# Performance work log

Measured on AMD Instinct MI355X. Metric: run time of the kernel, lower is better.

Reference implementation:

```python
import jax, jax.numpy as jnp
import numpy as np

SNUM = 8           # number of select-PUF stages
PUF_LEN = 64       # arbiter PUF length -> phi dim = PUF_LEN + 1
BATCH = 262144     # number of challenge-response pairs
D = 2 ** SNUM      # 256 combinations


def _make_kron_tables():
    """Replicates the W/B kron construction from combineMPUF.__init__.
    Returns Wmat, Bmat of shape [SNUM, D]; row i is W[i]/B[i] (originally [1, D])."""
    tmpX = np.array([[1], [1]])
    Ws, Bs = [], []
    for i in range(SNUM):
        w = np.array([[-1], [1]])
        b = np.array([[1], [0]])
        for _ in range(i + 1, SNUM):
            w = np.kron(tmpX, w)
            b = np.kron(tmpX, b)
        for _ in range(i):
            w = np.kron(w, tmpX)
            b = np.kron(b, tmpX)
        Ws.append(w.T[0])
        Bs.append(b.T[0])
    return (jnp.asarray(np.stack(Ws), jnp.float32),
            jnp.asarray(np.stack(Bs), jnp.float32))


def setup_inputs() -> dict:
    key = jax.random.key(0)
    k_phi, k_ws, k_bs, k_wd, k_bd = jax.random.split(key, 5)
    F = PUF_LEN + 1
    scale = 1.0 / np.sqrt(F)  # ~ torch Linear init scale
    phi = jax.random.normal(k_phi, (BATCH, F), dtype=jnp.float32)
    W_S = jax.random.uniform(k_ws, (SNUM, F), jnp.float32, -scale, scale)
    b_S = jax.random.uniform(k_bs, (SNUM,), jnp.float32, -scale, scale)
    W_D = jax.random.uniform(k_wd, (D, F), jnp.float32, -scale, scale)
    b_D = jax.random.uniform(k_bd, (D,), jnp.float32, -scale, scale)
    Wmat, Bmat = _make_kron_tables()
    return {"phi": phi, "W_S": W_S, "b_S": b_S, "W_D": W_D, "b_D": b_D,
            "Wmat": Wmat, "Bmat": Bmat}


def reference(phi, W_S, b_S, W_D, b_D, Wmat, Bmat):
    # phi: [B, F]; W_S: [SNUM, F]; W_D: [D, F]; Wmat/Bmat: [SNUM, D]
    Sdelta = phi @ W_S.T + b_S            # [B, SNUM]
    Ddelta = phi @ W_D.T + b_D            # [B, D]
    Souts = jax.nn.sigmoid(Sdelta)        # [B, SNUM]
    Douts = jax.nn.sigmoid(Ddelta)        # [B, D]
    # sigmoid-gated outer-product chain: M = prod_i (s_i * w_i + b_i)
    M = jnp.ones_like(Douts)
    for i in range(SNUM):                 # small fixed structural loop
        M = M * (Souts[:, i:i + 1] * Wmat[i] + Bmat[i])
    ans = jnp.sum(Douts * M * 0.99999, axis=-1, keepdims=True)  # [B, 1]
    reliability_output = jnp.abs(Sdelta)  # [B, SNUM]
    return ans, reliability_output
```

## Files before the change

kernel.cpp:

```cpp
#include <hip/hip_runtime.h>

typedef float  f32x4  __attribute__((ext_vector_type(4)));
typedef float  f32x4a __attribute__((ext_vector_type(4), aligned(4)));
typedef float  f32x2  __attribute__((ext_vector_type(2)));
typedef __bf16 bf16x8 __attribute__((ext_vector_type(8)));
typedef short  short8 __attribute__((ext_vector_type(8)));

#define F      65
#define NTT    17
#define KS3    3
#define RPB    128
#define NCHUNK (NTT*KS3*64)

__device__ __forceinline__ unsigned short f2bf(float f) {
  unsigned int u = __builtin_bit_cast(unsigned int, f);
  u += 0x7FFFu + ((u >> 16) & 1u);
  return (unsigned short)(u >> 16);
}
__device__ __forceinline__ float fast_sigmoid(float x) {
  float e = __builtin_amdgcn_exp2f(-1.4426950408889634f * x);
  return __builtin_amdgcn_rcpf(1.0f + e);
}
template<int CTRL>
__device__ __forceinline__ float dpp_mov(float v) {
  return __builtin_bit_cast(float,
    __builtin_amdgcn_update_dpp(0, __builtin_bit_cast(int, v), CTRL, 0xF, 0xF, true));
}

__global__ void prep_w(const float* __restrict__ W_S, const float* __restrict__ b_S,
                       const float* __restrict__ W_D, const float* __restrict__ b_D,
                       unsigned short* __restrict__ wsb) {
  int b = blockIdx.x;
  int t = b / 3, s = b % 3;
  int l = threadIdx.x;
  int c = l & 15, q = l >> 4;
  short8 out;
#pragma unroll
  for (int j = 0; j < 8; ++j) {
    int k = 32 * s + 8 * q + j;
    float v = 0.0f;
    if (t < 16) {
      int n = 16 * t + c;
      if (k < F)       v = W_D[n * F + k];
      else if (k == F) v = b_D[n];
    } else if (c < 8) {
      if (k < F)       v = W_S[c * F + k];
      else if (k == F) v = b_S[c];
    }
    out[j] = (short)f2bf(v);
  }
  reinterpret_cast<short8*>(wsb)[b * 64 + l] = out;
}

__launch_bounds__(512, 4)
__global__ void mpuf_main(const float* __restrict__ phi,
                          const unsigned short* __restrict__ wsb,
                          float* __restrict__ out_ans,
                          float* __restrict__ out_rel) {
  __shared__ short8 ldsB[NCHUNK];
  __shared__ float  soutv[RPB][10];
  __shared__ float  rowrec[RPB][18];

  const int tid  = threadIdx.x;
  const int wave = tid >> 6;
  const int l    = tid & 63;
  const int c    = l & 15;
  const int q    = l >> 4;
  const int wrow = wave * 16;
  const int brow = blockIdx.x * RPB;

  const float* prow = phi + (size_t)(brow + wrow + c) * F;

  f32x4a f4[4];
#pragma unroll
  for (int s = 0; s < 2; ++s) {
    f4[2 * s]     = *reinterpret_cast<const f32x4a*>(prow + 32 * s + 8 * q);
    f4[2 * s + 1] = *reinterpret_cast<const f32x4a*>(prow + 32 * s + 8 * q + 4);
  }
  const float a64 = prow[64];

  const short8* wsv = reinterpret_cast<const short8*>(wsb);
#pragma unroll
  for (int i = 0; i < 7; ++i) {
    int idx = tid + i * 512;
    if (idx < NCHUNK) ldsB[idx] = wsv[idx];
  }

  bf16x8 af[3];
#pragma unroll
  for (int s = 0; s < 2; ++s) {
    short8 ar;
#pragma unroll
    for (int j = 0; j < 4; ++j) {
      ar[j]     = (short)f2bf(f4[2 * s][j]);
      ar[j + 4] = (short)f2bf(f4[2 * s + 1][j]);
    }
    af[s] = __builtin_bit_cast(bf16x8, ar);
  }
  {
    short8 ar = {0, 0, 0, 0, 0, 0, 0, 0};
    if (q == 0) {
      ar[0] = (short)f2bf(a64);
      ar[1] = (short)0x3F80;
    }
    af[2] = __builtin_bit_cast(bf16x8, ar);
  }

  __syncthreads();

  f32x4 accS = {};
#pragma unroll
  for (int s = 0; s < KS3; ++s)
    accS = __builtin_amdgcn_mfma_f32_16x16x32_bf16(
               af[s], __builtin_bit_cast(bf16x8, ldsB[(16 * KS3 + s) * 64 + l]),
               accS, 0, 0, 0);

  if (c < 8) {
#pragma unroll
    for (int r = 0; r < 4; ++r) {
      const int R = wrow + q * 4 + r;
      float sd = accS[r];
      out_rel[(size_t)(brow + R) * 8 + c] = fabsf(sd);
      soutv[R][c] = fast_sigmoid(sd);
    }
  }

  float Ml[4];
#pragma unroll
  for (int r = 0; r < 4; ++r) {
    const int R = wrow + q * 4 + r;
    f32x2 p01 = *reinterpret_cast<const f32x2*>(&soutv[R][0]);
    f32x2 p23 = *reinterpret_cast<const f32x2*>(&soutv[R][2]);
    f32x2 p45 = *reinterpret_cast<const f32x2*>(&soutv[R][4]);
    f32x2 p67 = *reinterpret_cast<const f32x2*>(&soutv[R][6]);
    float m = 0.99999f;
    m *= (c & 1) ? p01[0] : 1.0f - p01[0];
    m *= (c & 2) ? p01[1] : 1.0f - p01[1];
    m *= (c & 4) ? p23[0] : 1.0f - p23[0];
    m *= (c & 8) ? p23[1] : 1.0f - p23[1];
    Ml[r] = m;
    float mt = (c & 1) ? p45[0] : 1.0f - p45[0];
    mt *= (c & 2) ? p45[1] : 1.0f - p45[1];
    mt *= (c & 4) ? p67[0] : 1.0f - p67[0];
    mt *= (c & 8) ? p67[1] : 1.0f - p67[1];
    rowrec[R][c] = mt;
  }

  float ansacc[4] = {0.0f, 0.0f, 0.0f, 0.0f};

#pragma unroll 1
  for (int tp = 0; tp < 8; ++tp) {
    const int t0 = 2 * tp, t1 = t0 + 1;
    f32x4 A0 = {}, A1 = {};
#pragma unroll
    for (int s = 0; s < KS3; ++s)
      A0 = __builtin_amdgcn_mfma_f32_16x16x32_bf16(
               af[s], __builtin_bit_cast(bf16x8, ldsB[(t0 * KS3 + s) * 64 + l]),
               A0, 0, 0, 0);
#pragma unroll
    for (int s = 0; s < KS3; ++s)
      A1 = __builtin_amdgcn_mfma_f32_16x16x32_bf16(
               af[s], __builtin_bit_cast(bf16x8, ldsB[(t1 * KS3 + s) * 64 + l]),
               A1, 0, 0, 0);
#pragma unroll
    for (int r = 0; r < 4; ++r) {
      const int R = wrow + q * 4 + r;
      f32x2 w = *reinterpret_cast<const f32x2*>(&rowrec[R][t0]);
      float d0 = fast_sigmoid(A0[r]);
      float d1 = fast_sigmoid(A1[r]);
      ansacc[r] = fmaf(d0, Ml[r] * w[0], ansacc[r]);
      ansacc[r] = fmaf(d1, Ml[r] * w[1], ansacc[r]);
    }
  }

#pragma unroll
  for (int r = 0; r < 4; ++r) {
    float v = ansacc[r];
    v += dpp_mov<0xB1>(v);
    v += dpp_mov<0x4E>(v);
    v += dpp_mov<0x141>(v);
    v += dpp_mov<0x140>(v);
    ansacc[r] = v;
  }
  if (c == 0) {
    f32x4 o = { ansacc[0], ansacc[1], ansacc[2], ansacc[3] };
    *reinterpret_cast<f32x4*>(&out_ans[brow + wrow + q * 4]) = o;
  }
}

extern "C" void kernel_launch(void* const* d_in, const int* in_sizes, int n_in,
                              void* d_out, int out_size, void* d_ws, size_t ws_size,
                              hipStream_t stream) {
  const float* phi = (const float*)d_in[0];
  const float* W_S = (const float*)d_in[1];
  const float* b_S = (const float*)d_in[2];
  const float* W_D = (const float*)d_in[3];
  const float* b_D = (const float*)d_in[4];
  const int rows = in_sizes[0] / F;
  unsigned short* wsb = (unsigned short*)d_ws;
  float* out_ans = (float*)d_out;
  float* out_rel = out_ans + rows;
  hipLaunchKernelGGL(prep_w, dim3(NTT * KS3), dim3(64), 0, stream,
                     W_S, b_S, W_D, b_D, wsb);
  hipLaunchKernelGGL(mpuf_main, dim3(rows / RPB), dim3(512), 0, stream,
                     phi, wsb, out_ans, out_rel);
}
```

Baseline: 40.47 us.

## Stream weights from global into registers and process two row tiles per wave

Drops the per-block LDS staging of the bf16 weight matrix and its barrier. Each wave now loads the weight fragments straight from global/L2 into registers, prefetching the next tile pair one iteration ahead. Each wave now covers 32 rows (two A tiles), so every B fragment feeds two MFMAs, and blocks shrink to 256 threads. Ml is multiplied once after the loop instead of inside it. The cost is more register pressure and repeated global weight reads per wave, which now rely on cache hits.

Result: slower. 43.23 us (+6.8%).

```diff
diff --git a/kernel.cpp b/kernel.cpp
--- a/kernel.cpp
+++ b/kernel.cpp
@@ -2,7 +2,7 @@
 
 typedef float  f32x4  __attribute__((ext_vector_type(4)));
 typedef float  f32x4a __attribute__((ext_vector_type(4), aligned(4)));
-typedef float  f32x2  __attribute__((ext_vector_type(2)));
+typedef float  f32x2a __attribute__((ext_vector_type(2), aligned(4)));
 typedef __bf16 bf16x8 __attribute__((ext_vector_type(8)));
 typedef short  short8 __attribute__((ext_vector_type(8)));
 
@@ -10,13 +10,7 @@
 #define NTT    17
 #define KS3    3
 #define RPB    128
-#define NCHUNK (NTT*KS3*64)
-
-__device__ __forceinline__ unsigned short f2bf(float f) {
-  unsigned int u = __builtin_bit_cast(unsigned int, f);
-  u += 0x7FFFu + ((u >> 16) & 1u);
-  return (unsigned short)(u >> 16);
-}
+
 __device__ __forceinline__ float fast_sigmoid(float x) {
   float e = __builtin_amdgcn_exp2f(-1.4426950408889634f * x);
   return __builtin_amdgcn_rcpf(1.0f + e);
@@ -25,6 +19,13 @@
 __device__ __forceinline__ float dpp_mov(float v) {
   return __builtin_bit_cast(float,
     __builtin_amdgcn_update_dpp(0, __builtin_bit_cast(int, v), CTRL, 0xF, 0xF, true));
+}
+__device__ __forceinline__ float reduce16(float v) {
+  v += dpp_mov<0xB1>(v);
+  v += dpp_mov<0x4E>(v);
+  v += dpp_mov<0x141>(v);
+  v += dpp_mov<0x140>(v);
+  return v;
 }
 
 __global__ void prep_w(const float* __restrict__ W_S, const float* __restrict__ b_S,
@@ -47,144 +48,159 @@
       if (k < F)       v = W_S[c * F + k];
       else if (k == F) v = b_S[c];
     }
-    out[j] = (short)f2bf(v);
+    unsigned int u = __builtin_bit_cast(unsigned int, v);
+    u += 0x7FFFu + ((u >> 16) & 1u);
+    out[j] = (short)(u >> 16);
   }
   reinterpret_cast<short8*>(wsb)[b * 64 + l] = out;
 }
 
-__launch_bounds__(512, 4)
+__device__ __forceinline__ float ml_mt(float (*soutv)[9], float (*rowrec)[17],
+                                       int R, int c) {
+  f32x2a p01 = *reinterpret_cast<const f32x2a*>(&soutv[R][0]);
+  f32x2a p23 = *reinterpret_cast<const f32x2a*>(&soutv[R][2]);
+  f32x2a p45 = *reinterpret_cast<const f32x2a*>(&soutv[R][4]);
+  f32x2a p67 = *reinterpret_cast<const f32x2a*>(&soutv[R][6]);
+  float m = 0.99999f;
+  m *= (c & 1) ? p01[0] : 1.0f - p01[0];
+  m *= (c & 2) ? p01[1] : 1.0f - p01[1];
+  m *= (c & 4) ? p23[0] : 1.0f - p23[0];
+  m *= (c & 8) ? p23[1] : 1.0f - p23[1];
+  float mt = (c & 1) ? p45[0] : 1.0f - p45[0];
+  mt *= (c & 2) ? p45[1] : 1.0f - p45[1];
+  mt *= (c & 4) ? p67[0] : 1.0f - p67[0];
+  mt *= (c & 8) ? p67[1] : 1.0f - p67[1];
+  rowrec[R][c] = mt;
+  return m;
+}
+
+__launch_bounds__(256, 4)
 __global__ void mpuf_main(const float* __restrict__ phi,
                           const unsigned short* __restrict__ wsb,
                           float* __restrict__ out_ans,
                           float* __restrict__ out_rel) {
-  __shared__ short8 ldsB[NCHUNK];
-  __shared__ float  soutv[RPB][10];
-  __shared__ float  rowrec[RPB][18];
+  __shared__ float soutv[RPB][9];
+  __shared__ float rowrec[RPB][17];
 
   const int tid  = threadIdx.x;
   const int wave = tid >> 6;
   const int l    = tid & 63;
   const int c    = l & 15;
   const int q    = l >> 4;
-  const int wrow = wave * 16;
+  const int wrow = wave * 32;
   const int brow = blockIdx.x * RPB;
 
-  const float* prow = phi + (size_t)(brow + wrow + c) * F;
-
-  f32x4a f4[4];
+  const float* prow0 = phi + (size_t)(brow + wrow + c) * F;
+  const float* prow1 = prow0 + (size_t)16 * F;
+
+  f32x4a f40[4], f41[4];
 #pragma unroll
   for (int s = 0; s < 2; ++s) {
-    f4[2 * s]     = *reinterpret_cast<const f32x4a*>(prow + 32 * s + 8 * q);
-    f4[2 * s + 1] = *reinterpret_cast<const f32x4a*>(prow + 32 * s + 8 * q + 4);
-  }
-  const float a64 = prow[64];
+    f40[2 * s]     = *reinterpret_cast<const f32x4a*>(prow0 + 32 * s + 8 * q);
+    f40[2 * s + 1] = *reinterpret_cast<const f32x4a*>(prow0 + 32 * s + 8 * q + 4);
+    f41[2 * s]     = *reinterpret_cast<const f32x4a*>(prow1 + 32 * s + 8 * q);
+    f41[2 * s + 1] = *reinterpret_cast<const f32x4a*>(prow1 + 32 * s + 8 * q + 4);
+  }
+  const float a640 = prow0[64];
+  const float a641 = prow1[64];
 
   const short8* wsv = reinterpret_cast<const short8*>(wsb);
-#pragma unroll
-  for (int i = 0; i < 7; ++i) {
-    int idx = tid + i * 512;
-    if (idx < NCHUNK) ldsB[idx] = wsv[idx];
-  }
-
-  bf16x8 af[3];
+  short8 bS[3], bcur[6];
+#pragma unroll
+  for (int s = 0; s < 3; ++s) bS[s] = wsv[(16 * KS3 + s) * 64 + l];
+#pragma unroll
+  for (int i = 0; i < 6; ++i) bcur[i] = wsv[i * 64 + l];
+
+  bf16x8 af0[3], af1[3];
 #pragma unroll
   for (int s = 0; s < 2; ++s) {
-    short8 ar;
+    bf16x8 v0, v1;
 #pragma unroll
     for (int j = 0; j < 4; ++j) {
-      ar[j]     = (short)f2bf(f4[2 * s][j]);
-      ar[j + 4] = (short)f2bf(f4[2 * s + 1][j]);
-    }
-    af[s] = __builtin_bit_cast(bf16x8, ar);
+      v0[j]     = (__bf16)f40[2 * s][j];
+      v0[j + 4] = (__bf16)f40[2 * s + 1][j];
+      v1[j]     = (__bf16)f41[2 * s][j];
+      v1[j + 4] = (__bf16)f41[2 * s + 1][j];
+    }
+    af0[s] = v0; af1[s] = v1;
   }
   {
-    short8 ar = {0, 0, 0, 0, 0, 0, 0, 0};
+    bf16x8 v0 = {}, v1 = {};
     if (q == 0) {
-      ar[0] = (short)f2bf(a64);
-      ar[1] = (short)0x3F80;
-    }
-    af[2] = __builtin_bit_cast(bf16x8, ar);
-  }
-
-  __syncthreads();
-
-  f32x4 accS = {};
-#pragma unroll
-  for (int s = 0; s < KS3; ++s)
-    accS = __builtin_amdgcn_mfma_f32_16x16x32_bf16(
-               af[s], __builtin_bit_cast(bf16x8, ldsB[(16 * KS3 + s) * 64 + l]),
-               accS, 0, 0, 0);
-
+      v0[0] = (__bf16)a640; v0[1] = (__bf16)1.0f;
+      v1[0] = (__bf16)a641; v1[1] = (__bf16)1.0f;
+    }
+    af0[2] = v0; af1[2] = v1;
+  }
+
+  f32x4 aS0 = {}, aS1 = {};
+#pragma unroll
+  for (int s = 0; s < KS3; ++s) {
+    bf16x8 b = __builtin_bit_cast(bf16x8, bS[s]);
+    aS0 = __builtin_amdgcn_mfma_f32_16x16x32_bf16(af0[s], b, aS0, 0, 0, 0);
+    aS1 = __builtin_amdgcn_mfma_f32_16x16x32_bf16(af1[s], b, aS1, 0, 0, 0);
+  }
   if (c < 8) {
 #pragma unroll
     for (int r = 0; r < 4; ++r) {
-      const int R = wrow + q * 4 + r;
-      float sd = accS[r];
-      out_rel[(size_t)(brow + R) * 8 + c] = fabsf(sd);
-      soutv[R][c] = fast_sigmoid(sd);
-    }
-  }
-
-  float Ml[4];
+      const int R0 = wrow + q * 4 + r, R1 = R0 + 16;
+      out_rel[(size_t)(brow + R0) * 8 + c] = fabsf(aS0[r]);
+      out_rel[(size_t)(brow + R1) * 8 + c] = fabsf(aS1[r]);
+      soutv[R0][c] = fast_sigmoid(aS0[r]);
+      soutv[R1][c] = fast_sigmoid(aS1[r]);
+    }
+  }
+
+  float Ml0[4], Ml1[4];
 #pragma unroll
   for (int r = 0; r < 4; ++r) {
-    const int R = wrow + q * 4 + r;
-    f32x2 p01 = *reinterpret_cast<const f32x2*>(&soutv[R][0]);
-    f32x2 p23 = *reinterpret_cast<const f32x2*>(&soutv[R][2]);
-    f32x2 p45 = *reinterpret_cast<const f32x2*>(&soutv[R][4]);
-    f32x2 p67 = *reinterpret_cast<const f32x2*>(&soutv[R][6]);
-    float m = 0.99999f;
-    m *= (c & 1) ? p01[0] : 1.0f - p01[0];
-    m *= (c & 2) ? p01[1] : 1.0f - p01[1];
-    m *= (c & 4) ? p23[0] : 1.0f - p23[0];
-    m *= (c & 8) ? p23[1] : 1.0f - p23[1];
-    Ml[r] = m;
-    float mt = (c & 1) ? p45[0] : 1.0f - p45[0];
-    mt *= (c & 2) ? p45[1] : 1.0f - p45[1];
-    mt *= (c & 4) ? p67[0] : 1.0f - p67[0];
-    mt *= (c & 8) ? p67[1] : 1.0f - p67[1];
-    rowrec[R][c] = mt;
-  }
-
-  float ansacc[4] = {0.0f, 0.0f, 0.0f, 0.0f};
+    const int R0 = wrow + q * 4 + r;
+    Ml0[r] = ml_mt(soutv, rowrec, R0, c);
+    Ml1[r] = ml_mt(soutv, rowrec, R0 + 16, c);
+  }
+
+  float ans0[4] = {0, 0, 0, 0}, ans1[4] = {0, 0, 0, 0};
 
 #pragma unroll 1
   for (int tp = 0; tp < 8; ++tp) {
-    const int t0 = 2 * tp, t1 = t0 + 1;
-    f32x4 A0 = {}, A1 = {};
-#pragma unroll
-    for (int s = 0; s < KS3; ++s)
-      A0 = __builtin_amdgcn_mfma_f32_16x16x32_bf16(
-               af[s], __builtin_bit_cast(bf16x8, ldsB[(t0 * KS3 + s) * 64 + l]),
-               A0, 0, 0, 0);
-#pragma unroll
-    for (int s = 0; s < KS3; ++s)
-      A1 = __builtin_amdgcn_mfma_f32_16x16x32_bf16(
-               af[s], __builtin_bit_cast(bf16x8, ldsB[(t1 * KS3 + s) * 64 + l]),
-               A1, 0, 0, 0);
+    f32x4 a00 = {}, a01 = {}, a10 = {}, a11 = {};
+#pragma unroll
+    for (int s = 0; s < KS3; ++s) {
+      bf16x8 b0 = __builtin_bit_cast(bf16x8, bcur[s]);
+      bf16x8 b1 = __builtin_bit_cast(bf16x8, bcur[3 + s]);
+      a00 = __builtin_amdgcn_mfma_f32_16x16x32_bf16(af0[s], b0, a00, 0, 0, 0);
+      a10 = __builtin_amdgcn_mfma_f32_16x16x32_bf16(af1[s], b0, a10, 0, 0, 0);
+      a01 = __builtin_amdgcn_mfma_f32_16x16x32_bf16(af0[s], b1, a01, 0, 0, 0);
+      a11 = __builtin_amdgcn_mfma_f32_16x16x32_bf16(af1[s], b1, a11, 0, 0, 0);
+    }
+    short8 bnxt[6];
+    const int tpn = (tp < 7) ? tp + 1 : 7;
+#pragma unroll
+    for (int i = 0; i < 6; ++i) bnxt[i] = wsv[(tpn * 6 + i) * 64 + l];
 #pragma unroll
     for (int r = 0; r < 4; ++r) {
-      const int R = wrow + q * 4 + r;
-      f32x2 w = *reinterpret_cast<const f32x2*>(&rowrec[R][t0]);
-      float d0 = fast_sigmoid(A0[r]);
-      float d1 = fast_sigmoid(A1[r]);
-      ansacc[r] = fmaf(d0, Ml[r] * w[0], ansacc[r]);
-      ansacc[r] = fmaf(d1, Ml[r] * w[1], ansacc[r]);
-    }
+      const int R0 = wrow + q * 4 + r, R1 = R0 + 16;
+      f32x2a w0 = *reinterpret_cast<const f32x2a*>(&rowrec[R0][2 * tp]);
+      f32x2a w1 = *reinterpret_cast<const f32x2a*>(&rowrec[R1][2 * tp]);
+      ans0[r] = fmaf(fast_sigmoid(a00[r]), w0[0], ans0[r]);
+      ans0[r] = fmaf(fast_sigmoid(a01[r]), w0[1], ans0[r]);
+      ans1[r] = fmaf(fast_sigmoid(a10[r]), w1[0], ans1[r]);
+      ans1[r] = fmaf(fast_sigmoid(a11[r]), w1[1], ans1[r]);
+    }
+#pragma unroll
+    for (int i = 0; i < 6; ++i) bcur[i] = bnxt[i];
   }
 
 #pragma unroll
   for (int r = 0; r < 4; ++r) {
-    float v = ansacc[r];
-    v += dpp_mov<0xB1>(v);
-    v += dpp_mov<0x4E>(v);
-    v += dpp_mov<0x141>(v);
-    v += dpp_mov<0x140>(v);
-    ansacc[r] = v;
+    ans0[r] = reduce16(Ml0[r] * ans0[r]);
+    ans1[r] = reduce16(Ml1[r] * ans1[r]);
   }
   if (c == 0) {
-    f32x4 o = { ansacc[0], ansacc[1], ansacc[2], ansacc[3] };
-    *reinterpret_cast<f32x4*>(&out_ans[brow + wrow + q * 4]) = o;
+    f32x4 o0 = { ans0[0], ans0[1], ans0[2], ans0[3] };
+    f32x4 o1 = { ans1[0], ans1[1], ans1[2], ans1[3] };
+    *reinterpret_cast<f32x4*>(&out_ans[brow + wrow + q * 4])      = o0;
+    *reinterpret_cast<f32x4*>(&out_ans[brow + wrow + 16 + q * 4]) = o1;
   }
 }
 
@@ -202,6 +218,6 @@
   float* out_rel = out_ans + rows;
   hipLaunchKernelGGL(prep_w, dim3(NTT * KS3), dim3(64), 0, stream,
                      W_S, b_S, W_D, b_D, wsb);
-  hipLaunchKernelGGL(mpuf_main, dim3(rows / RPB), dim3(512), 0, stream,
+  hipLaunchKernelGGL(mpuf_main, dim3(rows / RPB), dim3(256), 0, stream,
                      phi, wsb, out_ans, out_rel);
 }
```
